# Performance work log

Measured on AMD Instinct MI355X. Metric: run time of the kernel, lower is better.

The kernel has to match this reference:

```python
import jax, jax.numpy as jnp
import numpy as np

STATE_DIM = 128
ACT_DIM = 32
ENC_K = 10   # encoder_spine_dim
DEC_K = 10   # decoder_dim
H0, H1 = 2048, 2048
BATCH = 16384
MAX_ACTION = 1.0
STD0 = 0.3872983346207417  # sqrt(0.15)


def setup_inputs() -> dict:
    key = jax.random.key(0)
    ks = jax.random.split(key, 10)
    state = jax.random.normal(ks[0], (BATCH, STATE_DIM), dtype=jnp.float32)
    # encoder params: mean linspace over mean_range, std constant
    mean_enc = jnp.broadcast_to(jnp.linspace(-3.0, 3.0, ENC_K, dtype=jnp.float32),
                                (1, STATE_DIM, ENC_K))
    std_enc = jnp.full((1, STATE_DIM, ENC_K), STD0, dtype=jnp.float32)
    def lin(k, fan_in, fan_out):
        bound = 1.0 / np.sqrt(fan_in)
        k1, k2 = jax.random.split(k)
        W = jax.random.uniform(k1, (fan_out, fan_in), jnp.float32, -bound, bound)
        b = jax.random.uniform(k2, (fan_out,), jnp.float32, -bound, bound)
        return W, b
    W1, b1 = lin(ks[1], STATE_DIM * ENC_K, H0)
    W2, b2 = lin(ks[2], H0, H1)
    W3, b3 = lin(ks[3], H1, ACT_DIM * DEC_K)
    # grouped conv1d: weight [act_dim, 1, dec_k], bias [act_dim]
    bound = 1.0 / np.sqrt(DEC_K)
    Wd = jax.random.uniform(ks[4], (ACT_DIM, 1, DEC_K), jnp.float32, -bound, bound)
    bd = jax.random.uniform(ks[5], (ACT_DIM,), jnp.float32, -bound, bound)
    return {"state": state, "mean_enc": mean_enc, "std_enc": std_enc,
            "W1": W1, "b1": b1, "W2": W2, "b2": b2, "W3": W3, "b3": b3,
            "Wd": Wd, "bd": bd}


def reference(state, mean_enc, std_enc, W1, b1, W2, b2, W3, b3, Wd, bd):
    # Population-coding encoder: sigmoid((obs - mean)/std), flattened
    spine = jax.nn.sigmoid((state[:, :, None] - mean_enc) / std_enc)  # [B, D, K]
    spine = spine.reshape(state.shape[0], -1)                         # [B, D*K]
    a = jax.nn.relu(spine @ W1.T + b1)
    a = jax.nn.relu(a @ W2.T + b2)
    a = a @ W3.T + b3                                                 # [B, A*Kd]
    d = a.reshape(-1, ACT_DIM, DEC_K)                                 # [B, A, Kd]
    # grouped Conv1d with kernel == length => per-channel dot product
    raw = jnp.einsum('bak,ak->ba', d, Wd[:, 0, :]) + bd               # [B, A]
    return MAX_ACTION * jnp.tanh(raw)
```

## Files before the change

kernel.cpp:

```cpp
#include <hip/hip_runtime.h>
#include <hip/hip_bf16.h>
#include <stdint.h>

#define BATCH   16384
#define SDIM    128
#define ENCK    10
#define ADIM    32
#define DECK    10
#define HID     2048
#define KSPINE  1280

typedef __bf16 bf16x8 __attribute__((ext_vector_type(8)));
typedef float  f32x4  __attribute__((ext_vector_type(4)));

typedef __attribute__((address_space(1))) const void kGlobalVoid;
typedef __attribute__((address_space(3))) void       kLdsVoid;

__device__ __forceinline__ unsigned short f2b(float f) {
  union { float f; unsigned u; } v; v.f = f;
  unsigned r = v.u + 0x7fffu + ((v.u >> 16) & 1u);
  return (unsigned short)(r >> 16);
}

#define ENC_BLKS  40960
#define W1_BLKS   5120
#define W2_BLKS   8192
#define WEFF_BLKS 256

__global__ __launch_bounds__(256) void prep_kernel(
    const float* __restrict__ state, const float* __restrict__ mean,
    const float* __restrict__ stdv,
    const float* __restrict__ W1, const float* __restrict__ W2,
    const float* __restrict__ W3, const float* __restrict__ Wd,
    const float* __restrict__ b3, const float* __restrict__ bd,
    unsigned* __restrict__ spine, unsigned* __restrict__ W1b,
    unsigned* __restrict__ W2b, unsigned short* __restrict__ Weff,
    float* __restrict__ beff) {
  int b = blockIdx.x, t = threadIdx.x;
  if (b < ENC_BLKS) {
    int idx = b * 256 + t;
    int idx1 = (int)(((long long)idx * 0x66666667LL) >> 33);
    int kk = idx - idx1 * 5;
    int d  = idx1 & (SDIM - 1);
    float x = state[idx1];
    int mi = d * ENCK + kk * 2;
    float m0 = mean[mi], m1 = mean[mi + 1];
    float s0 = stdv[mi], s1 = stdv[mi + 1];
    float v0 = 1.f / (1.f + __expf((m0 - x) / s0));
    float v1 = 1.f / (1.f + __expf((m1 - x) / s1));
    spine[idx] = (unsigned)f2b(v0) | ((unsigned)f2b(v1) << 16);
  } else if (b < ENC_BLKS + W1_BLKS) {
    int i = (b - ENC_BLKS) * 256 + t;
    float2 v = reinterpret_cast<const float2*>(W1)[i];
    W1b[i] = (unsigned)f2b(v.x) | ((unsigned)f2b(v.y) << 16);
  } else if (b < ENC_BLKS + W1_BLKS + W2_BLKS) {
    int i = (b - ENC_BLKS - W1_BLKS) * 256 + t;
    float2 v = reinterpret_cast<const float2*>(W2)[i];
    W2b[i] = (unsigned)f2b(v.x) | ((unsigned)f2b(v.y) << 16);
  } else if (b < ENC_BLKS + W1_BLKS + W2_BLKS + WEFF_BLKS) {
    int idx = (b - ENC_BLKS - W1_BLKS - W2_BLKS) * 256 + t;
    int a = idx >> 11, j = idx & 2047;
    float s = 0.f;
#pragma unroll
    for (int k = 0; k < DECK; ++k)
      s += Wd[a * DECK + k] * W3[(size_t)(a * DECK + k) * HID + j];
    Weff[idx] = f2b(s);
  } else {
    if (t < ADIM) {
      float s = bd[t];
#pragma unroll
      for (int k = 0; k < DECK; ++k) s += Wd[t * DECK + k] * b3[t * DECK + k];
      beff[t] = s;
    }
  }
}

#define A0B 0
#define B0B 32768
#define A1B 65536
#define B1B 98304

#define FENCE asm volatile("" ::: "memory")
#define SB0 __builtin_amdgcn_sched_barrier(0)
#define BAR __builtin_amdgcn_s_barrier()
#define LGKM0 do { asm volatile("s_waitcnt lgkmcnt(0)" ::: "memory"); SB0; } while (0)

#define STAGE(BASEPTR, R0A, R0B, LDS0, LDS1, KT)                                             \
  __builtin_amdgcn_global_load_lds((kGlobalVoid*)((BASEPTR) + (size_t)((R0A) + rs) * K + (KT) + ce), \
                                   (kLdsVoid*)(smem + (LDS0) + t * 16), 16, 0, 0);           \
  __builtin_amdgcn_global_load_lds((kGlobalVoid*)((BASEPTR) + (size_t)((R0B) + rs) * K + (KT) + ce), \
                                   (kLdsVoid*)(smem + (LDS1) + t * 16), 16, 0, 0);

#define DS_AF(DST, ABASE, MPN)                                                               \
  _Pragma("unroll")                                                                          \
  for (int j2 = 0; j2 < 2; ++j2) {                                                           \
    _Pragma("unroll")                                                                        \
    for (int ks = 0; ks < 2; ++ks) {                                                         \
      int rowl = wr * 128 + (MPN) * 32 + j2 * 16 + lr;                                       \
      DST[j2][ks] = *reinterpret_cast<const bf16x8*>(                                        \
          smem + (ABASE) + rowl * 128 + ((((ks) << 6) | (kh << 4)) ^ swz));                  \
    }                                                                                        \
  }

#define DS_B2(DST, NP, BBASE)                                                                \
  _Pragma("unroll")                                                                          \
  for (int ks = 0; ks < 2; ++ks) {                                                           \
    int rowl = wc * 64 + (NP) * 16 + lr;                                                     \
    DST[NP][ks] = *reinterpret_cast<const bf16x8*>(                                          \
        smem + (BBASE) + rowl * 128 + ((((ks) << 6) | (kh << 4)) ^ swz));                    \
  }

#define DS_BF(DST, BBASE)                                                                    \
  _Pragma("unroll")                                                                          \
  for (int n = 0; n < 4; ++n) {                                                              \
    _Pragma("unroll")                                                                        \
    for (int ks = 0; ks < 2; ++ks) {                                                         \
      int rowl = wc * 64 + n * 16 + lr;                                                      \
      DST[n][ks] = *reinterpret_cast<const bf16x8*>(                                         \
          smem + (BBASE) + rowl * 128 + ((((ks) << 6) | (kh << 4)) ^ swz));                  \
    }                                                                                        \
  }

#define MFMA16(MP, AF, BF)                                                                   \
  _Pragma("unroll")                                                                          \
  for (int j2 = 0; j2 < 2; ++j2)                                                             \
    _Pragma("unroll")                                                                        \
    for (int n = 0; n < 4; ++n)                                                              \
      _Pragma("unroll")                                                                      \
      for (int ks = 0; ks < 2; ++ks)                                                         \
        acc[(MP) * 2 + j2][n] = __builtin_amdgcn_mfma_f32_16x16x32_bf16(                     \
            AF[j2][ks], BF[n][ks], acc[(MP) * 2 + j2][n], 0, 0, 0);

#define SGB_PHASE                                                                            \
  __builtin_amdgcn_sched_group_barrier(0x8, 2, 0);                                           \
  __builtin_amdgcn_sched_group_barrier(0x100, 1, 0);                                         \
  __builtin_amdgcn_sched_group_barrier(0x8, 2, 0);                                           \
  __builtin_amdgcn_sched_group_barrier(0x100, 1, 0);                                         \
  __builtin_amdgcn_sched_group_barrier(0x20, 2, 0);                                          \
  __builtin_amdgcn_sched_group_barrier(0x8, 3, 0);                                           \
  __builtin_amdgcn_sched_group_barrier(0x100, 1, 0);                                         \
  __builtin_amdgcn_sched_group_barrier(0x8, 3, 0);                                           \
  __builtin_amdgcn_sched_group_barrier(0x100, 1, 0);                                         \
  __builtin_amdgcn_sched_group_barrier(0x8, 3, 0);                                           \
  __builtin_amdgcn_sched_group_barrier(0x100, 1, 0);                                         \
  __builtin_amdgcn_sched_group_barrier(0x8, 3, 0);                                           \
  __builtin_amdgcn_sched_group_barrier(0x100, 1, 0);

#define VM_NONE
#define VM2 asm volatile("s_waitcnt vmcnt(2)" ::: "memory"); SB0;
#define VM6 asm volatile("s_waitcnt vmcnt(6)" ::: "memory"); SB0;

#define PH(MP, AF_C, AF_N, BF_C, BF_N, NXT_A, NXT_MP, BBASE_N, VMW, STG)                     \
  do {                                                                                       \
    LGKM0;                                                                                   \
    VMW                                                                                      \
    __builtin_amdgcn_s_setprio(1);                                                           \
    MFMA16(MP, AF_C, BF_C);                                                                  \
    __builtin_amdgcn_s_setprio(0);                                                           \
    DS_AF(AF_N, NXT_A, NXT_MP);                                                              \
    DS_B2(BF_N, MP, BBASE_N);                                                                \
    STG;                                                                                     \
    SGB_PHASE;                                                                               \
    FENCE;                                                                                   \
    BAR;                                                                                     \
  } while (0)

__global__ __launch_bounds__(512, 2) void gemm256(
    const unsigned short* __restrict__ A,
    const unsigned short* __restrict__ Bw,
    const float* __restrict__ bias,
    unsigned short* __restrict__ Cout,
    int K, int NI) {
  __shared__ char smem[131072];

  const int t    = threadIdx.x;
  const int lane = t & 63;
  const int w    = t >> 6;
  const int wr   = w >> 2;
  const int wc   = w & 3;
  const int lr   = lane & 15;
  const int kh   = lane >> 4;
  const int swz  = (lr & 7) << 4;
  const int rs   = t >> 3;
  const int ce   = ((t & 7) ^ (rs & 7)) << 3;

  const int bid = blockIdx.x;
  const int xcd = bid & 7, idx = bid >> 3;
  const int row0 = (xcd * 8 + (idx >> 3)) * 256;
  const int col0 = (idx & 7) * 256;

  f32x4 acc[8][4];
#pragma unroll
  for (int m = 0; m < 8; ++m)
#pragma unroll
    for (int n = 0; n < 4; ++n)
      acc[m][n] = (f32x4){0.f, 0.f, 0.f, 0.f};

  bf16x8 afc[2][2], afn[2][2], bfA[4][2], bfB[4][2];

  STAGE(Bw, col0 + 0,   col0 + 64,  B0B + 0,     B0B + 8192,  0);
  STAGE(Bw, col0 + 128, col0 + 192, B0B + 16384, B0B + 24576, 0);
  STAGE(A,  row0 + 0,   row0 + 128, A0B + 0,     A0B + 16384, 0);
  STAGE(A,  row0 + 64,  row0 + 192, A0B + 8192,  A0B + 24576, 0);
  STAGE(Bw, col0 + 0,   col0 + 64,  B1B + 0,     B1B + 8192,  64);
  STAGE(Bw, col0 + 128, col0 + 192, B1B + 16384, B1B + 24576, 64);
  STAGE(A,  row0 + 0,   row0 + 128, A1B + 0,     A1B + 16384, 64);
  asm volatile("s_waitcnt vmcnt(0)" ::: "memory");
  FENCE; BAR;
  DS_AF(afc, A0B, 0);
  DS_BF(bfA, B0B);

  for (int i = 0; i < NI; ++i) {
    int kt0 = i << 7;
    int kt1 = kt0 + 64;
    int kt2 = kt0 + 128; if (kt2 >= K) kt2 -= K;
    int kt3 = kt0 + 192; if (kt3 >= K) kt3 -= K;

    PH(0, afc, afn, bfA, bfB, A0B, 1, B1B, VM2,
       STAGE(A,  row0 + 64,  row0 + 192, A1B + 8192,  A1B + 24576, kt1));
    PH(1, afn, afc, bfA, bfB, A0B, 2, B1B, VM_NONE,
       STAGE(Bw, col0 + 0,   col0 + 64,  B0B + 0,     B0B + 8192,  kt2));
    PH(2, afc, afn, bfA, bfB, A0B, 3, B1B, VM_NONE,
       STAGE(Bw, col0 + 128, col0 + 192, B0B + 16384, B0B + 24576, kt2));
    PH(3, afn, afc, bfA, bfB, A1B, 0, B1B, VM6,
       STAGE(A,  row0 + 0,   row0 + 128, A0B + 0,     A0B + 16384, kt2));
    PH(0, afc, afn, bfB, bfA, A1B, 1, B0B, VM2,
       STAGE(A,  row0 + 64,  row0 + 192, A0B + 8192,  A0B + 24576, kt2));
    PH(1, afn, afc, bfB, bfA, A1B, 2, B0B, VM_NONE,
       STAGE(Bw, col0 + 0,   col0 + 64,  B1B + 0,     B1B + 8192,  kt3));
    PH(2, afc, afn, bfB, bfA, A1B, 3, B0B, VM_NONE,
       STAGE(Bw, col0 + 128, col0 + 192, B1B + 16384, B1B + 24576, kt3));
    PH(3, afn, afc, bfB, bfA, A0B, 0, B0B, VM6,
       STAGE(A,  row0 + 0,   row0 + 128, A1B + 0,     A1B + 16384, kt3));
  }

#pragma unroll
  for (int m = 0; m < 8; ++m) {
    int gr0 = row0 + wr * 128 + m * 16 + kh * 4;
#pragma unroll
    for (int n = 0; n < 4; ++n) {
      int gc = col0 + wc * 64 + n * 16 + lr;
      float bv = bias[gc];
#pragma unroll
      for (int v = 0; v < 4; ++v) {
        float val = fmaxf(acc[m][n][v] + bv, 0.f);
        Cout[(size_t)(gr0 + v) * 2048 + gc] = f2b(val);
      }
    }
  }
}

__global__ __launch_bounds__(256) void gemm_skinny(
    const unsigned short* __restrict__ A,
    const unsigned short* __restrict__ Bw,
    const float* __restrict__ beff,
    float* __restrict__ out) {
  __shared__ char red[6144];
  const int t = threadIdx.x, lane = t & 63, w = t >> 6;
  const int lr = lane & 15, kh = lane >> 4;
  const int row0 = blockIdx.x * 16;
  const int kb = w * (HID / 4);
  f32x4 acc[2];
  acc[0] = (f32x4){0.f, 0.f, 0.f, 0.f};
  acc[1] = (f32x4){0.f, 0.f, 0.f, 0.f};

  const unsigned short* Arow = A  + (size_t)(row0 + lr) * HID + kb + kh * 8;
  const unsigned short* B0   = Bw + (size_t)(lr) * HID + kb + kh * 8;
  const unsigned short* B1   = Bw + (size_t)(16 + lr) * HID + kb + kh * 8;

#pragma unroll 4
  for (int kt = 0; kt < HID / 4; kt += 32) {
    bf16x8 a  = *reinterpret_cast<const bf16x8*>(Arow + kt);
    bf16x8 b0 = *reinterpret_cast<const bf16x8*>(B0 + kt);
    bf16x8 b1 = *reinterpret_cast<const bf16x8*>(B1 + kt);
    acc[0] = __builtin_amdgcn_mfma_f32_16x16x32_bf16(a, b0, acc[0], 0, 0, 0);
    acc[1] = __builtin_amdgcn_mfma_f32_16x16x32_bf16(a, b1, acc[1], 0, 0, 0);
  }

  if (w) {
    char* p = red + (w - 1) * 2048 + lane * 32;
    *reinterpret_cast<f32x4*>(p)      = acc[0];
    *reinterpret_cast<f32x4*>(p + 16) = acc[1];
  }
  __syncthreads();
  if (w == 0) {
#pragma unroll
    for (int j = 0; j < 3; ++j) {
      char* p = red + j * 2048 + lane * 32;
      acc[0] += *reinterpret_cast<const f32x4*>(p);
      acc[1] += *reinterpret_cast<const f32x4*>(p + 16);
    }
#pragma unroll
    for (int n = 0; n < 2; ++n)
#pragma unroll
      for (int v = 0; v < 4; ++v) {
        int row = row0 + kh * 4 + v;
        int col = n * 16 + lr;
        out[(size_t)row * ADIM + col] = tanhf(acc[n][v] + beff[col]);
      }
  }
}

extern "C" void kernel_launch(void* const* d_in, const int* in_sizes, int n_in,
                              void* d_out, int out_size, void* d_ws, size_t ws_size,
                              hipStream_t stream) {
  const float* state    = (const float*)d_in[0];
  const float* mean_enc = (const float*)d_in[1];
  const float* std_enc  = (const float*)d_in[2];
  const float* W1 = (const float*)d_in[3];
  const float* b1 = (const float*)d_in[4];
  const float* W2 = (const float*)d_in[5];
  const float* b2 = (const float*)d_in[6];
  const float* W3 = (const float*)d_in[7];
  const float* b3 = (const float*)d_in[8];
  const float* Wd = (const float*)d_in[9];
  const float* bd = (const float*)d_in[10];

  char* ws = (char*)d_ws;
  unsigned*       W1b   = (unsigned*)(ws + 0);
  unsigned*       W2b   = (unsigned*)(ws + 5242880);
  unsigned short* Weff  = (unsigned short*)(ws + 13631488);
  float*          beff  = (float*)(ws + 13762560);
  unsigned*       spine = (unsigned*)(ws + 13762688);
  unsigned short* h1    = (unsigned short*)(ws + 55705728);
  unsigned short* h2    = (unsigned short*)(ws + 122814592);

  prep_kernel<<<ENC_BLKS + W1_BLKS + W2_BLKS + WEFF_BLKS + 1, 256, 0, stream>>>(
      state, mean_enc, std_enc, W1, W2, W3, Wd, b3, bd,
      spine, W1b, W2b, Weff, beff);

  gemm256<<<512, 512, 0, stream>>>((const unsigned short*)spine, (const unsigned short*)W1b,
                                   b1, h1, KSPINE, KSPINE / 128);
  gemm256<<<512, 512, 0, stream>>>(h1, (const unsigned short*)W2b, b2, h2, HID, HID / 128);
  gemm_skinny<<<BATCH / 16, 256, 0, stream>>>(h2, Weff, beff, (float*)d_out);
}
```

Measured before the change: 242.6 us.

## Fuse decoder skinny GEMM into second GEMM epilogue with split-N partials

The second hidden-layer GEMM now keeps its ReLU'd bf16 tile in LDS and immediately multiplies it by the folded decoder weights. Each of the 8 column blocks writes a partial 32-wide output, and a small reduce kernel sums them and applies tanh. This removes the 64MB h2 write and re-read and the separate skinny GEMM pass. W1 and W2 rows are permuted so each lane owns 4 consecutive output columns, which lets the epilogue use packed 8-byte stores. The cost is an extra 16MB partial buffer and a fourth kernel launch.

```diff
diff --git a/kernel.cpp b/kernel.cpp
--- a/kernel.cpp
+++ b/kernel.cpp
@@ -20,6 +20,11 @@
   union { float f; unsigned u; } v; v.f = f;
   unsigned r = v.u + 0x7fffu + ((v.u >> 16) & 1u);
   return (unsigned short)(r >> 16);
+}
+
+__device__ __forceinline__ int permrow(int pr) {
+  int q = pr & 63;
+  return (pr & ~63) | (((q & 15) << 2) | (q >> 4));
 }
 
 #define ENC_BLKS  40960
@@ -51,11 +56,13 @@
     spine[idx] = (unsigned)f2b(v0) | ((unsigned)f2b(v1) << 16);
   } else if (b < ENC_BLKS + W1_BLKS) {
     int i = (b - ENC_BLKS) * 256 + t;
-    float2 v = reinterpret_cast<const float2*>(W1)[i];
+    int row = i / 640, c2 = i - row * 640;
+    float2 v = reinterpret_cast<const float2*>(W1)[permrow(row) * 640 + c2];
     W1b[i] = (unsigned)f2b(v.x) | ((unsigned)f2b(v.y) << 16);
   } else if (b < ENC_BLKS + W1_BLKS + W2_BLKS) {
     int i = (b - ENC_BLKS - W1_BLKS) * 256 + t;
-    float2 v = reinterpret_cast<const float2*>(W2)[i];
+    int row = i >> 10, c2 = i & 1023;
+    float2 v = reinterpret_cast<const float2*>(W2)[permrow(row) * 1024 + c2];
     W2b[i] = (unsigned)f2b(v.x) | ((unsigned)f2b(v.y) << 16);
   } else if (b < ENC_BLKS + W1_BLKS + W2_BLKS + WEFF_BLKS) {
     int idx = (b - ENC_BLKS - W1_BLKS - W2_BLKS) * 256 + t;
@@ -165,140 +172,163 @@
     BAR;                                                                                     \
   } while (0)
 
-__global__ __launch_bounds__(512, 2) void gemm256(
-    const unsigned short* __restrict__ A,
-    const unsigned short* __restrict__ Bw,
-    const float* __restrict__ bias,
-    unsigned short* __restrict__ Cout,
+#define GEMM_BODY                                                                            \
+  __shared__ char smem[131072];                                                              \
+  const int t    = threadIdx.x;                                                              \
+  const int lane = t & 63;                                                                   \
+  const int w    = t >> 6;                                                                   \
+  const int wr   = w >> 2;                                                                   \
+  const int wc   = w & 3;                                                                    \
+  const int lr   = lane & 15;                                                                \
+  const int kh   = lane >> 4;                                                                \
+  const int swz  = (lr & 7) << 4;                                                            \
+  const int rs   = t >> 3;                                                                   \
+  const int ce   = ((t & 7) ^ (rs & 7)) << 3;                                                \
+  const int bid = blockIdx.x;                                                                \
+  const int xcd = bid & 7, idx = bid >> 3;                                                   \
+  const int row0 = (xcd * 8 + (idx >> 3)) * 256;                                             \
+  const int col0 = (idx & 7) * 256;                                                          \
+  f32x4 acc[8][4];                                                                           \
+  _Pragma("unroll")                                                                          \
+  for (int m = 0; m < 8; ++m)                                                                \
+    _Pragma("unroll")                                                                        \
+    for (int n = 0; n < 4; ++n)                                                              \
+      acc[m][n] = (f32x4){0.f, 0.f, 0.f, 0.f};                                               \
+  bf16x8 afc[2][2], afn[2][2], bfA[4][2], bfB[4][2];                                         \
+  STAGE(Bw, col0 + 0,   col0 + 64,  B0B + 0,     B0B + 8192,  0);                            \
+  STAGE(Bw, col0 + 128, col0 + 192, B0B + 16384, B0B + 24576, 0);                            \
+  STAGE(A,  row0 + 0,   row0 + 128, A0B + 0,     A0B + 16384, 0);                            \
+  STAGE(A,  row0 + 64,  row0 + 192, A0B + 8192,  A0B + 24576, 0);                            \
+  STAGE(Bw, col0 + 0,   col0 + 64,  B1B + 0,     B1B + 8192,  64);                           \
+  STAGE(Bw, col0 + 128, col0 + 192, B1B + 16384, B1B + 24576, 64);                           \
+  STAGE(A,  row0 + 0,   row0 + 128, A1B + 0,     A1B + 16384, 64);                           \
+  asm volatile("s_waitcnt vmcnt(0)" ::: "memory");                                           \
+  FENCE; BAR;                                                                                \
+  DS_AF(afc, A0B, 0);                                                                        \
+  DS_BF(bfA, B0B);                                                                           \
+  for (int i = 0; i < NI; ++i) {                                                             \
+    int kt0 = i << 7;                                                                        \
+    int kt1 = kt0 + 64;                                                                      \
+    int kt2 = kt0 + 128; if (kt2 >= K) kt2 -= K;                                             \
+    int kt3 = kt0 + 192; if (kt3 >= K) kt3 -= K;                                             \
+    PH(0, afc, afn, bfA, bfB, A0B, 1, B1B, VM2,                                              \
+       STAGE(A,  row0 + 64,  row0 + 192, A1B + 8192,  A1B + 24576, kt1));                    \
+    PH(1, afn, afc, bfA, bfB, A0B, 2, B1B, VM_NONE,                                          \
+       STAGE(Bw, col0 + 0,   col0 + 64,  B0B + 0,     B0B + 8192,  kt2));                    \
+    PH(2, afc, afn, bfA, bfB, A0B, 3, B1B, VM_NONE,                                          \
+       STAGE(Bw, col0 + 128, col0 + 192, B0B + 16384, B0B + 24576, kt2));                    \
+    PH(3, afn, afc, bfA, bfB, A1B, 0, B1B, VM6,                                              \
+       STAGE(A,  row0 + 0,   row0 + 128, A0B + 0,     A0B + 16384, kt2));                    \
+    PH(0, afc, afn, bfB, bfA, A1B, 1, B0B, VM2,                                              \
+       STAGE(A,  row0 + 64,  row0 + 192, A0B + 8192,  A0B + 24576, kt2));                    \
+    PH(1, afn, afc, bfB, bfA, A1B, 2, B0B, VM_NONE,                                          \
+       STAGE(Bw, col0 + 0,   col0 + 64,  B1B + 0,     B1B + 8192,  kt3));                    \
+    PH(2, afc, afn, bfB, bfA, A1B, 3, B0B, VM_NONE,                                          \
+       STAGE(Bw, col0 + 128, col0 + 192, B1B + 16384, B1B + 24576, kt3));                    \
+    PH(3, afn, afc, bfB, bfA, A0B, 0, B0B, VM6,                                              \
+       STAGE(A,  row0 + 0,   row0 + 128, A1B + 0,     A1B + 16384, kt3));                    \
+  }
+
+__global__ __launch_bounds__(512, 2) void gemm_h1(
+    const unsigned short* __restrict__ A, const unsigned short* __restrict__ Bw,
+    const float* __restrict__ bias, unsigned short* __restrict__ Cout,
     int K, int NI) {
-  __shared__ char smem[131072];
-
-  const int t    = threadIdx.x;
-  const int lane = t & 63;
-  const int w    = t >> 6;
-  const int wr   = w >> 2;
-  const int wc   = w & 3;
-  const int lr   = lane & 15;
-  const int kh   = lane >> 4;
-  const int swz  = (lr & 7) << 4;
-  const int rs   = t >> 3;
-  const int ce   = ((t & 7) ^ (rs & 7)) << 3;
-
-  const int bid = blockIdx.x;
-  const int xcd = bid & 7, idx = bid >> 3;
-  const int row0 = (xcd * 8 + (idx >> 3)) * 256;
-  const int col0 = (idx & 7) * 256;
-
-  f32x4 acc[8][4];
-#pragma unroll
-  for (int m = 0; m < 8; ++m)
-#pragma unroll
-    for (int n = 0; n < 4; ++n)
-      acc[m][n] = (f32x4){0.f, 0.f, 0.f, 0.f};
-
-  bf16x8 afc[2][2], afn[2][2], bfA[4][2], bfB[4][2];
-
-  STAGE(Bw, col0 + 0,   col0 + 64,  B0B + 0,     B0B + 8192,  0);
-  STAGE(Bw, col0 + 128, col0 + 192, B0B + 16384, B0B + 24576, 0);
-  STAGE(A,  row0 + 0,   row0 + 128, A0B + 0,     A0B + 16384, 0);
-  STAGE(A,  row0 + 64,  row0 + 192, A0B + 8192,  A0B + 24576, 0);
-  STAGE(Bw, col0 + 0,   col0 + 64,  B1B + 0,     B1B + 8192,  64);
-  STAGE(Bw, col0 + 128, col0 + 192, B1B + 16384, B1B + 24576, 64);
-  STAGE(A,  row0 + 0,   row0 + 128, A1B + 0,     A1B + 16384, 64);
-  asm volatile("s_waitcnt vmcnt(0)" ::: "memory");
-  FENCE; BAR;
-  DS_AF(afc, A0B, 0);
-  DS_BF(bfA, B0B);
-
-  for (int i = 0; i < NI; ++i) {
-    int kt0 = i << 7;
-    int kt1 = kt0 + 64;
-    int kt2 = kt0 + 128; if (kt2 >= K) kt2 -= K;
-    int kt3 = kt0 + 192; if (kt3 >= K) kt3 -= K;
-
-    PH(0, afc, afn, bfA, bfB, A0B, 1, B1B, VM2,
-       STAGE(A,  row0 + 64,  row0 + 192, A1B + 8192,  A1B + 24576, kt1));
-    PH(1, afn, afc, bfA, bfB, A0B, 2, B1B, VM_NONE,
-       STAGE(Bw, col0 + 0,   col0 + 64,  B0B + 0,     B0B + 8192,  kt2));
-    PH(2, afc, afn, bfA, bfB, A0B, 3, B1B, VM_NONE,
-       STAGE(Bw, col0 + 128, col0 + 192, B0B + 16384, B0B + 24576, kt2));
-    PH(3, afn, afc, bfA, bfB, A1B, 0, B1B, VM6,
-       STAGE(A,  row0 + 0,   row0 + 128, A0B + 0,     A0B + 16384, kt2));
-    PH(0, afc, afn, bfB, bfA, A1B, 1, B0B, VM2,
-       STAGE(A,  row0 + 64,  row0 + 192, A0B + 8192,  A0B + 24576, kt2));
-    PH(1, afn, afc, bfB, bfA, A1B, 2, B0B, VM_NONE,
-       STAGE(Bw, col0 + 0,   col0 + 64,  B1B + 0,     B1B + 8192,  kt3));
-    PH(2, afc, afn, bfB, bfA, A1B, 3, B0B, VM_NONE,
-       STAGE(Bw, col0 + 128, col0 + 192, B1B + 16384, B1B + 24576, kt3));
-    PH(3, afn, afc, bfB, bfA, A0B, 0, B0B, VM6,
-       STAGE(A,  row0 + 0,   row0 + 128, A1B + 0,     A1B + 16384, kt3));
-  }
+  GEMM_BODY
 
 #pragma unroll
   for (int m = 0; m < 8; ++m) {
     int gr0 = row0 + wr * 128 + m * 16 + kh * 4;
-#pragma unroll
-    for (int n = 0; n < 4; ++n) {
-      int gc = col0 + wc * 64 + n * 16 + lr;
-      float bv = bias[gc];
+    int cb  = col0 + wc * 64 + lr * 4;
+    float bv0 = bias[cb], bv1 = bias[cb + 1], bv2 = bias[cb + 2], bv3 = bias[cb + 3];
+#pragma unroll
+    for (int v = 0; v < 4; ++v) {
+      unsigned lo = (unsigned)f2b(fmaxf(acc[m][0][v] + bv0, 0.f)) |
+                    ((unsigned)f2b(fmaxf(acc[m][1][v] + bv1, 0.f)) << 16);
+      unsigned hi = (unsigned)f2b(fmaxf(acc[m][2][v] + bv2, 0.f)) |
+                    ((unsigned)f2b(fmaxf(acc[m][3][v] + bv3, 0.f)) << 16);
+      *reinterpret_cast<uint2*>(&Cout[(size_t)(gr0 + v) * 2048 + cb]) = make_uint2(lo, hi);
+    }
+  }
+}
+
+__global__ __launch_bounds__(512, 2) void gemm_dec(
+    const unsigned short* __restrict__ A, const unsigned short* __restrict__ Bw,
+    const float* __restrict__ bias, const unsigned short* __restrict__ Weff,
+    float* __restrict__ out_part) {
+  const int K = HID, NI = HID / 128;
+  GEMM_BODY
+
+  asm volatile("s_waitcnt vmcnt(0)" ::: "memory");
+  LGKM0;
+  FENCE; BAR;
+
+#pragma unroll
+  for (int m = 0; m < 8; ++m) {
+    int r0  = wr * 128 + m * 16 + kh * 4;
+    int cbl = wc * 64 + lr * 4;
+    float bv0 = bias[col0 + cbl], bv1 = bias[col0 + cbl + 1];
+    float bv2 = bias[col0 + cbl + 2], bv3 = bias[col0 + cbl + 3];
+#pragma unroll
+    for (int v = 0; v < 4; ++v) {
+      int r = r0 + v;
+      unsigned lo = (unsigned)f2b(fmaxf(acc[m][0][v] + bv0, 0.f)) |
+                    ((unsigned)f2b(fmaxf(acc[m][1][v] + bv1, 0.f)) << 16);
+      unsigned hi = (unsigned)f2b(fmaxf(acc[m][2][v] + bv2, 0.f)) |
+                    ((unsigned)f2b(fmaxf(acc[m][3][v] + bv3, 0.f)) << 16);
+      int byte = r * 512 + ((cbl * 2) ^ ((r & 7) << 4));
+      *reinterpret_cast<uint2*>(smem + byte) = make_uint2(lo, hi);
+    }
+  }
+  FENCE; BAR;
+
+  f32x4 acc2[2][2];
+#pragma unroll
+  for (int mf = 0; mf < 2; ++mf)
+#pragma unroll
+    for (int nf = 0; nf < 2; ++nf) acc2[mf][nf] = (f32x4){0.f, 0.f, 0.f, 0.f};
+
+#pragma unroll
+  for (int kt = 0; kt < 256; kt += 32) {
+    bf16x8 aF[2], bF[2];
+#pragma unroll
+    for (int mf = 0; mf < 2; ++mf) {
+      int r = w * 32 + mf * 16 + lr;
+      aF[mf] = *reinterpret_cast<const bf16x8*>(
+          smem + r * 512 + (((kt + kh * 8) * 2) ^ ((r & 7) << 4)));
+    }
+#pragma unroll
+    for (int nf = 0; nf < 2; ++nf)
+      bF[nf] = *reinterpret_cast<const bf16x8*>(
+          Weff + (size_t)(nf * 16 + lr) * HID + col0 + kt + kh * 8);
+#pragma unroll
+    for (int mf = 0; mf < 2; ++mf)
+#pragma unroll
+      for (int nf = 0; nf < 2; ++nf)
+        acc2[mf][nf] = __builtin_amdgcn_mfma_f32_16x16x32_bf16(aF[mf], bF[nf], acc2[mf][nf], 0, 0, 0);
+  }
+
+  const int nb = idx & 7;
+  float* op = out_part + (size_t)nb * BATCH * ADIM;
+#pragma unroll
+  for (int mf = 0; mf < 2; ++mf)
+#pragma unroll
+    for (int nf = 0; nf < 2; ++nf)
 #pragma unroll
       for (int v = 0; v < 4; ++v) {
-        float val = fmaxf(acc[m][n][v] + bv, 0.f);
-        Cout[(size_t)(gr0 + v) * 2048 + gc] = f2b(val);
+        int r = w * 32 + mf * 16 + kh * 4 + v;
+        int a = nf * 16 + lr;
+        op[(size_t)(row0 + r) * ADIM + a] = acc2[mf][nf][v];
       }
-    }
-  }
-}
-
-__global__ __launch_bounds__(256) void gemm_skinny(
-    const unsigned short* __restrict__ A,
-    const unsigned short* __restrict__ Bw,
-    const float* __restrict__ beff,
+}
+
+__global__ __launch_bounds__(256) void reduce_tanh(
+    const float* __restrict__ part, const float* __restrict__ beff,
     float* __restrict__ out) {
-  __shared__ char red[6144];
-  const int t = threadIdx.x, lane = t & 63, w = t >> 6;
-  const int lr = lane & 15, kh = lane >> 4;
-  const int row0 = blockIdx.x * 16;
-  const int kb = w * (HID / 4);
-  f32x4 acc[2];
-  acc[0] = (f32x4){0.f, 0.f, 0.f, 0.f};
-  acc[1] = (f32x4){0.f, 0.f, 0.f, 0.f};
-
-  const unsigned short* Arow = A  + (size_t)(row0 + lr) * HID + kb + kh * 8;
-  const unsigned short* B0   = Bw + (size_t)(lr) * HID + kb + kh * 8;
-  const unsigned short* B1   = Bw + (size_t)(16 + lr) * HID + kb + kh * 8;
-
-#pragma unroll 4
-  for (int kt = 0; kt < HID / 4; kt += 32) {
-    bf16x8 a  = *reinterpret_cast<const bf16x8*>(Arow + kt);
-    bf16x8 b0 = *reinterpret_cast<const bf16x8*>(B0 + kt);
-    bf16x8 b1 = *reinterpret_cast<const bf16x8*>(B1 + kt);
-    acc[0] = __builtin_amdgcn_mfma_f32_16x16x32_bf16(a, b0, acc[0], 0, 0, 0);
-    acc[1] = __builtin_amdgcn_mfma_f32_16x16x32_bf16(a, b1, acc[1], 0, 0, 0);
-  }
-
-  if (w) {
-    char* p = red + (w - 1) * 2048 + lane * 32;
-    *reinterpret_cast<f32x4*>(p)      = acc[0];
-    *reinterpret_cast<f32x4*>(p + 16) = acc[1];
-  }
-  __syncthreads();
-  if (w == 0) {
-#pragma unroll
-    for (int j = 0; j < 3; ++j) {
-      char* p = red + j * 2048 + lane * 32;
-      acc[0] += *reinterpret_cast<const f32x4*>(p);
-      acc[1] += *reinterpret_cast<const f32x4*>(p + 16);
-    }
-#pragma unroll
-    for (int n = 0; n < 2; ++n)
-#pragma unroll
-      for (int v = 0; v < 4; ++v) {
-        int row = row0 + kh * 4 + v;
-        int col = n * 16 + lr;
-        out[(size_t)row * ADIM + col] = tanhf(acc[n][v] + beff[col]);
-      }
-  }
+  int i = blockIdx.x * 256 + threadIdx.x;
+  float s = beff[i & 31];
+#pragma unroll
+  for (int nb = 0; nb < 8; ++nb) s += part[(size_t)nb * BATCH * ADIM + i];
+  out[i] = tanhf(s);
 }
 
 extern "C" void kernel_launch(void* const* d_in, const int* in_sizes, int n_in,
@@ -323,14 +353,14 @@
   float*          beff  = (float*)(ws + 13762560);
   unsigned*       spine = (unsigned*)(ws + 13762688);
   unsigned short* h1    = (unsigned short*)(ws + 55705728);
-  unsigned short* h2    = (unsigned short*)(ws + 122814592);
+  float*          part  = (float*)(ws + 122814592);
 
   prep_kernel<<<ENC_BLKS + W1_BLKS + W2_BLKS + WEFF_BLKS + 1, 256, 0, stream>>>(
       state, mean_enc, std_enc, W1, W2, W3, Wd, b3, bd,
       spine, W1b, W2b, Weff, beff);
 
-  gemm256<<<512, 512, 0, stream>>>((const unsigned short*)spine, (const unsigned short*)W1b,
+  gemm_h1<<<512, 512, 0, stream>>>((const unsigned short*)spine, (const unsigned short*)W1b,
                                    b1, h1, KSPINE, KSPINE / 128);
-  gemm256<<<512, 512, 0, stream>>>(h1, (const unsigned short*)W2b, b2, h2, HID, HID / 128);
-  gemm_skinny<<<BATCH / 16, 256, 0, stream>>>(h2, Weff, beff, (float*)d_out);
-}
+  gemm_dec<<<512, 512, 0, stream>>>(h1, (const unsigned short*)W2b, b2, Weff, part);
+  reduce_tanh<<<(BATCH * ADIM) / 256, 256, 0, stream>>>(part, beff, (float*)d_out);
+}
```

Measured after the change: 233.2 us. 3.9% less time.
